# Optimization experiments

Hardware: AMD Instinct MI355X
Metric: run time of the kernel (lower is better)

## Reference

```python
import jax, jax.numpy as jnp
import numpy as np

L, N = 200, 256  # event_list_length, num_nodes


def setup_inputs() -> dict:
    key = jax.random.key(0)
    ks = jax.random.split(key, 7)
    time = jax.random.uniform(ks[0], (2,), dtype=jnp.float32)
    event_list = jax.random.normal(ks[1], (L + 1, N, N), dtype=jnp.float32)
    u_begin = jax.random.uniform(ks[2], (N, N, 3), dtype=jnp.float32)
    # xavier-ish scales for params
    a = jax.random.normal(ks[3], (L, N, N, 3), dtype=jnp.float32) * 0.05
    w = jax.random.normal(ks[4], (L, N, 1, N), dtype=jnp.float32) * 0.05
    liner_w = jax.random.normal(ks[5], (N, 3), dtype=jnp.float32) * 0.5
    liner_b = jax.random.normal(ks[6], (N,), dtype=jnp.float32) * 0.1
    return {"time": time, "event_list": event_list, "u_begin": u_begin,
            "a": a, "w": w, "liner_w": liner_w, "liner_b": liner_b,
            "batch_size": 2}


def reference(time, event_list, u_begin, a, w, liner_w, liner_b, batch_size):
    # event_list[:-1]; consumed in pairs (start, start+1) with batch_size == 2
    T = event_list.shape[0] - 1
    S = T // batch_size                      # number of scan steps
    n = event_list.shape[1]
    e2 = event_list[:T].reshape(S, 2, n, n)          # [S,2,N,N]
    a2 = a[:T].reshape(S, 2, n, n, 3)                # [S,2,N,N,3]
    w2 = w[:T, :, 0, :].reshape(S, 2, n, n)          # [S,2,N,N] (squeeze the 1-dim)
    t0, t1 = time[0], time[1]                        # original always uses time[0], time[1]

    def step(u, xs):
        ep, ap, wp = xs                              # [2,N,N], [2,N,N,3], [2,N,N]
        # per-node scalar dot: w[start][node] @ event_begin[k][node]
        dot0 = jnp.einsum('nk,nk->n', wp[0], ep[0])  # [N]
        dot1 = jnp.einsum('nk,nk->n', wp[1], ep[1])
        # math.exp in the original returns a Python float -> constant w.r.t. autograd
        f0 = jax.lax.stop_gradient(jnp.exp(-dot0 * t0))[:, None, None]
        f1 = jax.lax.stop_gradient(jnp.exp(-dot1 * t1))[:, None, None]
        lamda = u + ap[0] * f0 + ap[1] * f1          # [N,N,3]
        temp = jax.nn.softmax(lamda, axis=-1)        # softmax over the 3-dim (dim=1 of [N,3] per node)
        # per-node Linear(3,1): temp[node] @ W_node^T + b_node -> [N,N]
        out = jnp.einsum('nmc,nc->nm', temp, liner_w) + liner_b[:, None]
        # state update was .detach().cpu().numpy() -> stop_gradient
        return jax.lax.stop_gradient(temp), out

    _, outs = jax.lax.scan(step, u_begin, (e2, a2, w2))
    return outs                                      # [S, N, N] == [T/2, N, N]
```

## Files before the change

### kernel.cpp

```cpp
#include <hip/hip_runtime.h>


#define NN 256
#define TT 200
#define SS 100
#define CH 10
#define SLABS (2*CH)
#define HALF 128
#define SEG (HALF*3)
#define CHUNKF (SLABS*SEG)
#define NCHUNK (SS/CH)

typedef const __attribute__((address_space(1))) void* gas1;
typedef __attribute__((address_space(3))) void* las3;

__global__ __launch_bounds__(256) void f_kernel(
    const float* __restrict__ timep,
    const float* __restrict__ ev,
    const float* __restrict__ w,
    float* __restrict__ fs)
{
    const int lane  = threadIdx.x & 63;
    const int gwave = blockIdx.x * 4 + (threadIdx.x >> 6);
    const int n  = gwave & 255;
    const int tp = gwave >> 8;
    const int ta = 2 * tp;

    const size_t ro_a = (size_t)ta * (NN * NN) + (size_t)n * NN;
    const size_t ro_b = ro_a + (size_t)(NN * NN);
    float4 wa = ((const float4*)(w  + ro_a))[lane];
    float4 ea = ((const float4*)(ev + ro_a))[lane];
    float4 wb = ((const float4*)(w  + ro_b))[lane];
    float4 eb = ((const float4*)(ev + ro_b))[lane];
    float da = wa.x * ea.x;
    da = fmaf(wa.y, ea.y, da); da = fmaf(wa.z, ea.z, da); da = fmaf(wa.w, ea.w, da);
    float db = wb.x * eb.x;
    db = fmaf(wb.y, eb.y, db); db = fmaf(wb.z, eb.z, db); db = fmaf(wb.w, eb.w, db);
#pragma unroll
    for (int off = 1; off < 64; off <<= 1) {
        da += __shfl_xor(da, off, 64);
        db += __shfl_xor(db, off, 64);
    }
    if (lane == 0) {
        float2 r;
        r.x = __expf(-da * timep[0]);
        r.y = __expf(-db * timep[1]);
        ((float2*)(fs + (size_t)n * TT))[tp] = r;
    }
}

__global__ __launch_bounds__(HALF) void scan_kernel(
    const float* __restrict__ fs_g,
    const float* __restrict__ ub,
    const float* __restrict__ a,
    const float* __restrict__ lw,
    const float* __restrict__ lb,
    float* __restrict__ out)
{
    __shared__ float fs[TT];
    __shared__ float buf[2][CHUNKF];

    const int nb   = blockIdx.x >> 1;
    const int h    = blockIdx.x & 1;
    const int mm   = threadIdx.x;
    const int lane = mm & 63;
    const int wid  = mm >> 6;

    if (mm < TT) fs[mm] = fs_g[(size_t)nb * TT + mm];
    if (mm + HALF < TT) fs[mm + HALF] = fs_g[(size_t)nb * TT + mm + HALF];

    const size_t rowbase = (size_t)nb * 768 + (size_t)h * SEG;
    const size_t TS = (size_t)NN * NN * 3;

    auto fill = [&](int c, int which) {
#pragma unroll
        for (int r = 0; r < 15; ++r) {
            const unsigned base4 = (unsigned)((r * 2 + wid) * 64);
            const unsigned q  = base4 + (unsigned)lane;
            const unsigned tl = q / 96;
            const unsigned o4 = q - tl * 96;
            const float* g = a + (size_t)(c * SLABS + tl) * TS + rowbase + (size_t)o4 * 4;
            float* l = &buf[which][(size_t)base4 * 4];
            __builtin_amdgcn_global_load_lds((gas1)g, (las3)l, 16, 0, 0);
        }
    };

    fill(0, 0);

    float u0, u1, u2;
    {
        const size_t b = rowbase + (size_t)mm * 3;
        u0 = ub[b + 0]; u1 = ub[b + 1]; u2 = ub[b + 2];
    }
    const float w0 = lw[nb * 3 + 0];
    const float w1 = lw[nb * 3 + 1];
    const float w2 = lw[nb * 3 + 2];
    const float bbias = lb[nb];
    float* op = out + (size_t)nb * NN + (size_t)h * HALF + mm;

    __syncthreads();

    for (int c = 0; c < NCHUNK; ++c) {
        if (c + 1 < NCHUNK) fill(c + 1, (c + 1) & 1);
        const float* B = buf[c & 1];
#pragma unroll
        for (int k = 0; k < CH; ++k) {
            const int s = c * CH + k;
            const float* s0 = B + (size_t)(2 * k) * SEG + (size_t)mm * 3;
            const float* s1 = s0 + SEG;
            const float f0 = fs[2 * s];
            const float f1 = fs[2 * s + 1];
            float l0 = fmaf(s0[0], f0, fmaf(s1[0], f1, u0));
            float l1 = fmaf(s0[1], f0, fmaf(s1[1], f1, u1));
            float l2 = fmaf(s0[2], f0, fmaf(s1[2], f1, u2));
            float mx = fmaxf(l0, fmaxf(l1, l2));
            float e0 = __expf(l0 - mx);
            float e1 = __expf(l1 - mx);
            float e2 = __expf(l2 - mx);
            float inv = __builtin_amdgcn_rcpf(e0 + e1 + e2);
            u0 = e0 * inv; u1 = e1 * inv; u2 = e2 * inv;
            op[(size_t)s * (NN * NN)] = fmaf(u0, w0, fmaf(u1, w1, fmaf(u2, w2, bbias)));
        }
        __syncthreads();
    }
}

extern "C" void kernel_launch(void* const* d_in, const int* in_sizes, int n_in,
                              void* d_out, int out_size, void* d_ws, size_t ws_size,
                              hipStream_t stream) {
    const float* timep = (const float*)d_in[0];
    const float* ev    = (const float*)d_in[1];
    const float* ub    = (const float*)d_in[2];
    const float* a     = (const float*)d_in[3];
    const float* w     = (const float*)d_in[4];
    const float* lw    = (const float*)d_in[5];
    const float* lb    = (const float*)d_in[6];
    float* out = (float*)d_out;
    float* fs  = (float*)d_ws;

    f_kernel<<<(SS * NN) / 4, 256, 0, stream>>>(timep, ev, w, fs);
    scan_kernel<<<2 * NN, HALF, 0, stream>>>(fs, ub, a, lw, lb, out);
}
```

Before: 309.3 us.

## Split scan across quarter-row blocks with register-staged prefetch and one compute wave

```diff
diff --git a/kernel.cpp b/kernel.cpp
--- a/kernel.cpp
+++ b/kernel.cpp
@@ -6,13 +6,11 @@
 #define SS 100
 #define CH 10
 #define SLABS (2*CH)
-#define HALF 128
-#define SEG (HALF*3)
-#define CHUNKF (SLABS*SEG)
+#define NCH 64
+#define SLAB_F (NCH*3)
+#define CHUNK_F (SLABS*SLAB_F)
+#define CHUNK_F4 (CHUNK_F/4)
 #define NCHUNK (SS/CH)
-
-typedef const __attribute__((address_space(1))) void* gas1;
-typedef __attribute__((address_space(3))) void* las3;
 
 __global__ __launch_bounds__(256) void f_kernel(
     const float* __restrict__ timep,
@@ -24,9 +22,8 @@
     const int gwave = blockIdx.x * 4 + (threadIdx.x >> 6);
     const int n  = gwave & 255;
     const int tp = gwave >> 8;
-    const int ta = 2 * tp;
 
-    const size_t ro_a = (size_t)ta * (NN * NN) + (size_t)n * NN;
+    const size_t ro_a = (size_t)(2 * tp) * (NN * NN) + (size_t)n * NN;
     const size_t ro_b = ro_a + (size_t)(NN * NN);
     float4 wa = ((const float4*)(w  + ro_a))[lane];
     float4 ea = ((const float4*)(ev + ro_a))[lane];
@@ -49,7 +46,7 @@
     }
 }
 
-__global__ __launch_bounds__(HALF) void scan_kernel(
+__global__ __launch_bounds__(256) void scan_kernel(
     const float* __restrict__ fs_g,
     const float* __restrict__ ub,
     const float* __restrict__ a,
@@ -58,69 +55,85 @@
     float* __restrict__ out)
 {
     __shared__ float fs[TT];
-    __shared__ float buf[2][CHUNKF];
+    __shared__ float buf[2][CHUNK_F];
 
-    const int nb   = blockIdx.x >> 1;
-    const int h    = blockIdx.x & 1;
-    const int mm   = threadIdx.x;
-    const int lane = mm & 63;
-    const int wid  = mm >> 6;
+    const int nb  = blockIdx.x >> 2;
+    const int qt  = blockIdx.x & 3;
+    const int tid = threadIdx.x;
 
-    if (mm < TT) fs[mm] = fs_g[(size_t)nb * TT + mm];
-    if (mm + HALF < TT) fs[mm + HALF] = fs_g[(size_t)nb * TT + mm + HALF];
+    if (tid < TT) fs[tid] = fs_g[(size_t)nb * TT + tid];
 
-    const size_t rowbase = (size_t)nb * 768 + (size_t)h * SEG;
+    const size_t rowbase = (size_t)nb * 768 + (size_t)qt * SLAB_F;
     const size_t TS = (size_t)NN * NN * 3;
 
-    auto fill = [&](int c, int which) {
-#pragma unroll
-        for (int r = 0; r < 15; ++r) {
-            const unsigned base4 = (unsigned)((r * 2 + wid) * 64);
-            const unsigned q  = base4 + (unsigned)lane;
-            const unsigned tl = q / 96;
-            const unsigned o4 = q - tl * 96;
-            const float* g = a + (size_t)(c * SLABS + tl) * TS + rowbase + (size_t)o4 * 4;
-            float* l = &buf[which][(size_t)base4 * 4];
-            __builtin_amdgcn_global_load_lds((gas1)g, (las3)l, 16, 0, 0);
+    float4 pf0, pf1, pf2, pf3;
+    auto load_chunk = [&](int c) {
+        const int q0 = tid, q1 = tid + 256, q2 = tid + 512, q3 = tid + 768;
+        {
+            const int tl = q0 / 48, o4 = q0 - tl * 48;
+            pf0 = *(const float4*)(a + (size_t)(c * SLABS + tl) * TS + rowbase + (size_t)o4 * 4);
+        }
+        {
+            const int tl = q1 / 48, o4 = q1 - tl * 48;
+            pf1 = *(const float4*)(a + (size_t)(c * SLABS + tl) * TS + rowbase + (size_t)o4 * 4);
+        }
+        {
+            const int tl = q2 / 48, o4 = q2 - tl * 48;
+            pf2 = *(const float4*)(a + (size_t)(c * SLABS + tl) * TS + rowbase + (size_t)o4 * 4);
+        }
+        if (q3 < CHUNK_F4) {
+            const int tl = q3 / 48, o4 = q3 - tl * 48;
+            pf3 = *(const float4*)(a + (size_t)(c * SLABS + tl) * TS + rowbase + (size_t)o4 * 4);
         }
     };
+    auto store_chunk = [&](int which) {
+        float4* B = (float4*)buf[which];
+        B[tid]       = pf0;
+        B[tid + 256] = pf1;
+        B[tid + 512] = pf2;
+        if (tid + 768 < CHUNK_F4) B[tid + 768] = pf3;
+    };
 
-    fill(0, 0);
+    float u0 = 0.f, u1 = 0.f, u2 = 0.f, w0 = 0.f, w1 = 0.f, w2 = 0.f, bbias = 0.f;
+    float* op = out;
+    if (tid < NCH) {
+        const size_t b = rowbase + (size_t)tid * 3;
+        u0 = ub[b + 0]; u1 = ub[b + 1]; u2 = ub[b + 2];
+        w0 = lw[nb * 3 + 0]; w1 = lw[nb * 3 + 1]; w2 = lw[nb * 3 + 2];
+        bbias = lb[nb];
+        op = out + (size_t)nb * NN + (size_t)qt * NCH + tid;
+    }
 
-    float u0, u1, u2;
-    {
-        const size_t b = rowbase + (size_t)mm * 3;
-        u0 = ub[b + 0]; u1 = ub[b + 1]; u2 = ub[b + 2];
-    }
-    const float w0 = lw[nb * 3 + 0];
-    const float w1 = lw[nb * 3 + 1];
-    const float w2 = lw[nb * 3 + 2];
-    const float bbias = lb[nb];
-    float* op = out + (size_t)nb * NN + (size_t)h * HALF + mm;
-
+    load_chunk(0);
+    store_chunk(0);
     __syncthreads();
 
     for (int c = 0; c < NCHUNK; ++c) {
-        if (c + 1 < NCHUNK) fill(c + 1, (c + 1) & 1);
-        const float* B = buf[c & 1];
+        if (c + 1 < NCHUNK) load_chunk(c + 1);
+
+        if (tid < NCH) {
+            const float* B = buf[c & 1];
 #pragma unroll
-        for (int k = 0; k < CH; ++k) {
-            const int s = c * CH + k;
-            const float* s0 = B + (size_t)(2 * k) * SEG + (size_t)mm * 3;
-            const float* s1 = s0 + SEG;
-            const float f0 = fs[2 * s];
-            const float f1 = fs[2 * s + 1];
-            float l0 = fmaf(s0[0], f0, fmaf(s1[0], f1, u0));
-            float l1 = fmaf(s0[1], f0, fmaf(s1[1], f1, u1));
-            float l2 = fmaf(s0[2], f0, fmaf(s1[2], f1, u2));
-            float mx = fmaxf(l0, fmaxf(l1, l2));
-            float e0 = __expf(l0 - mx);
-            float e1 = __expf(l1 - mx);
-            float e2 = __expf(l2 - mx);
-            float inv = __builtin_amdgcn_rcpf(e0 + e1 + e2);
-            u0 = e0 * inv; u1 = e1 * inv; u2 = e2 * inv;
-            op[(size_t)s * (NN * NN)] = fmaf(u0, w0, fmaf(u1, w1, fmaf(u2, w2, bbias)));
+            for (int k = 0; k < CH; ++k) {
+                const int s = c * CH + k;
+                const float* s0 = B + (size_t)(2 * k) * SLAB_F + (size_t)tid * 3;
+                const float* s1 = s0 + SLAB_F;
+                const float f0 = fs[2 * s];
+                const float f1 = fs[2 * s + 1];
+                float l0 = fmaf(s0[0], f0, fmaf(s1[0], f1, u0));
+                float l1 = fmaf(s0[1], f0, fmaf(s1[1], f1, u1));
+                float l2 = fmaf(s0[2], f0, fmaf(s1[2], f1, u2));
+                float mx = fmaxf(l0, fmaxf(l1, l2));
+                float e0 = __expf(l0 - mx);
+                float e1 = __expf(l1 - mx);
+                float e2 = __expf(l2 - mx);
+                float inv = __builtin_amdgcn_rcpf(e0 + e1 + e2);
+                u0 = e0 * inv; u1 = e1 * inv; u2 = e2 * inv;
+                op[(size_t)s * (NN * NN)] = fmaf(u0, w0, fmaf(u1, w1, fmaf(u2, w2, bbias)));
+            }
         }
+
+        if (c + 1 < NCHUNK) store_chunk((c + 1) & 1);
         __syncthreads();
     }
 }
@@ -139,5 +152,5 @@
     float* fs  = (float*)d_ws;
 
     f_kernel<<<(SS * NN) / 4, 256, 0, stream>>>(timep, ev, w, fs);
-    scan_kernel<<<2 * NN, HALF, 0, stream>>>(fs, ub, a, lw, lb, out);
+    scan_kernel<<<4 * NN, 256, 0, stream>>>(fs, ub, a, lw, lb, out);
 }
```

Result: no change. 307.1 us (-0.7%).
